# Kernel tuning notes

Measured on AMD Instinct MI355X. Metric: run time of the kernel, lower is better.

The kernel has to match this reference:

```python
import jax, jax.numpy as jnp
import numpy as np

N_NODES = 100000
N_EDGES = 1250000
D_FEAT = 64


def setup_inputs() -> dict:
    key = jax.random.key(0)
    kx, ke = jax.random.split(key)
    x = jax.random.normal(kx, (N_NODES, D_FEAT), dtype=jnp.float32)
    edge_index = jax.random.randint(ke, (2, N_EDGES), 0, N_NODES, dtype=jnp.int64)
    return {"x": x, "edge_index": edge_index}


def reference(x, edge_index):
    # propagate: scatter_nested gathers x[idxj] grouped by destination idxi
    # (a ragged per-node neighbor set); the module's sum_nested reduces each
    # group. Expressed densely and jit-ably as gather + segment-sum.
    idxi = edge_index[0, :]  # destination nodes
    idxj = edge_index[1, :]  # source nodes
    messages = x[idxj]  # [E, D] edge-level gather (memory-bound)
    out = jax.ops.segment_sum(messages, idxi, num_segments=N_NODES)  # [N, D]
    return out
```

## Files before the change

### kernel.cpp

```cpp
#include <hip/hip_runtime.h>

#define N_NODES 100000
#define N_EDGES 1250000
#define D_FEAT  64

#define NPB     256
#define NBINS   ((N_NODES + NPB - 1) / NPB)
#define BCAP    4096
#define EPB     4096
#define K1B     ((N_EDGES + EPB - 1) / EPB)
#define OVF_CAP 32768

#define CAP     48


__global__ __launch_bounds__(512) void k1_bin_kernel(
        const int* __restrict__ idxi, const int* __restrict__ idxj,
        int* __restrict__ gcursor, int* __restrict__ ovfcnt,
        int* __restrict__ ovf, int* __restrict__ binbuf) {
    __shared__ int hist[512];
    __shared__ int runstart[512];
    __shared__ int gbase[NBINS];
    __shared__ int cur[NBINS];
    __shared__ int staged[EPB];
    __shared__ unsigned short sbin[EPB];
    int t = threadIdx.x;
    hist[t] = 0;
    __syncthreads();

    long long base = (long long)blockIdx.x * EPB;
    int d[8], s[8], bn[8];
#pragma unroll
    for (int j = 0; j < 8; ++j) {
        long long e = base + t + j * 512;
        if (e < N_EDGES) {
            d[j] = idxi[e];
            s[j] = idxj[e];
            bn[j] = d[j] >> 8;
            atomicAdd(&hist[bn[j]], 1);
        } else {
            bn[j] = -1;
        }
    }
    __syncthreads();

    runstart[t] = hist[t];
    __syncthreads();
    for (int off = 1; off < 512; off <<= 1) {
        int add = (t >= off) ? runstart[t - off] : 0;
        __syncthreads();
        runstart[t] += add;
        __syncthreads();
    }
    int excl = runstart[t] - hist[t];
    __syncthreads();
    runstart[t] = excl;
    if (t < NBINS) {
        gbase[t] = hist[t] ? atomicAdd(&gcursor[t], hist[t]) : 0;
        cur[t] = 0;
    }
    __syncthreads();

#pragma unroll
    for (int j = 0; j < 8; ++j) {
        if (bn[j] >= 0) {
            int lofs = atomicAdd(&cur[bn[j]], 1);
            int idx = runstart[bn[j]] + lofs;
            staged[idx] = ((d[j] & 255) << 17) | s[j];
            sbin[idx] = (unsigned short)bn[j];
        }
    }
    __syncthreads();

    long long rem = (long long)N_EDGES - base;
    int n = (rem < EPB) ? (int)rem : EPB;
    for (int i = t; i < n; i += 512) {
        int b = sbin[i];
        int p = staged[i];
        int tgt = gbase[b] + (i - runstart[b]);
        if (tgt < BCAP) {
            binbuf[(size_t)b * BCAP + tgt] = p;
        } else {
            int op = atomicAdd(ovfcnt, 1);
            if (op < OVF_CAP) { ovf[2 * op] = b * NPB + (p >> 17); ovf[2 * op + 1] = p & 0x1FFFF; }
        }
    }
}

__global__ __launch_bounds__(1024) void k23_fused_kernel(
        const float* __restrict__ x, const int* __restrict__ gcursor,
        const int* __restrict__ binbuf, float* __restrict__ out) {
    __shared__ int cnt[NPB];
    __shared__ int excl[NPB];
    __shared__ int cur[NPB];
    __shared__ int stmp[NPB];
    __shared__ int srt[BCAP];
    int bin = blockIdx.x;
    int t = threadIdx.x;
    if (t < NPB) cnt[t] = 0;
    __syncthreads();

    int n = gcursor[bin];
    if (n > BCAP) n = BCAP;
    const int* src = binbuf + (size_t)bin * BCAP;
    int p[4];
#pragma unroll
    for (int j = 0; j < 4; ++j) {
        int i = t + j * 1024;
        p[j] = (i < n) ? src[i] : -1;
        if (p[j] >= 0) atomicAdd(&cnt[p[j] >> 17], 1);
    }
    __syncthreads();

    if (t < NPB) stmp[t] = cnt[t];
    __syncthreads();
    for (int off = 1; off < NPB; off <<= 1) {
        int v = 0;
        if (t < NPB && t >= off) v = stmp[t - off];
        __syncthreads();
        if (t < NPB) stmp[t] += v;
        __syncthreads();
    }
    if (t < NPB) {
        excl[t] = stmp[t] - cnt[t];
        cur[t] = 0;
    }
    __syncthreads();

#pragma unroll
    for (int j = 0; j < 4; ++j) {
        if (p[j] >= 0) {
            int dl = p[j] >> 17;
            int pos = excl[dl] + atomicAdd(&cur[dl], 1);
            srt[pos] = p[j] & 0x1FFFF;
        }
    }
    __syncthreads();

    int wave = t >> 6;
    int lane = t & 63;
    int sub  = lane >> 4;
    int c4   = lane & 15;
    for (int i = 0; i < 16; ++i) {
        int dloc = wave * 16 + i;
        int node = bin * NPB + dloc;
        if (node >= N_NODES) break;
        int base = excl[dloc];
        int l = cnt[dloc];
        float4 acc = make_float4(0.f, 0.f, 0.f, 0.f);
        int k = 0;
        for (; k + 8 <= l; k += 8) {
            int s0 = srt[base + k + sub];
            int s1 = srt[base + k + 4 + sub];
            const float4 v0 = *(const float4*)(x + (size_t)s0 * D_FEAT + c4 * 4);
            const float4 v1 = *(const float4*)(x + (size_t)s1 * D_FEAT + c4 * 4);
            acc.x += v0.x + v1.x;
            acc.y += v0.y + v1.y;
            acc.z += v0.z + v1.z;
            acc.w += v0.w + v1.w;
        }
        if (k + 4 <= l) {
            int s0 = srt[base + k + sub];
            const float4 v0 = *(const float4*)(x + (size_t)s0 * D_FEAT + c4 * 4);
            acc.x += v0.x; acc.y += v0.y; acc.z += v0.z; acc.w += v0.w;
            k += 4;
        }
        if (k + sub < l) {
            int s0 = srt[base + k + sub];
            const float4 v0 = *(const float4*)(x + (size_t)s0 * D_FEAT + c4 * 4);
            acc.x += v0.x; acc.y += v0.y; acc.z += v0.z; acc.w += v0.w;
        }

        acc.x += __shfl_xor(acc.x, 16, 64);
        acc.y += __shfl_xor(acc.y, 16, 64);
        acc.z += __shfl_xor(acc.z, 16, 64);
        acc.w += __shfl_xor(acc.w, 16, 64);
        acc.x += __shfl_xor(acc.x, 32, 64);
        acc.y += __shfl_xor(acc.y, 32, 64);
        acc.z += __shfl_xor(acc.z, 32, 64);
        acc.w += __shfl_xor(acc.w, 32, 64);

        if (lane < 16) {
            ((float4*)out)[(size_t)node * 16 + c4] = acc;
        }
    }
}

__global__ __launch_bounds__(256) void ovf_fixup_kernel(
        const float* __restrict__ x, const int* __restrict__ ovfcnt,
        const int* __restrict__ ovf, float* __restrict__ out) {
    int n = *ovfcnt;
    if (n > OVF_CAP) n = OVF_CAP;
    long long total = (long long)n * 16;
    long long stride = (long long)gridDim.x * blockDim.x;
    for (long long t = blockIdx.x * blockDim.x + threadIdx.x; t < total; t += stride) {
        int e  = (int)(t >> 4);
        int fo = ((int)t & 15) << 2;
        int d = ovf[2 * e];
        int s = ovf[2 * e + 1];
        const float4 v = *(const float4*)(x + (size_t)s * D_FEAT + fo);
        float* o = out + (size_t)d * D_FEAT + fo;
        atomicAdd(o + 0, v.x);
        atomicAdd(o + 1, v.y);
        atomicAdd(o + 2, v.z);
        atomicAdd(o + 3, v.w);
    }
}


__global__ __launch_bounds__(256) void scatter_pad_kernel(
        const int* __restrict__ idxi, const int* __restrict__ idxj,
        int* __restrict__ cnt, int* __restrict__ ovfcnt,
        int* __restrict__ ovf, int* __restrict__ bucket) {
    int e = blockIdx.x * blockDim.x + threadIdx.x;
    if (e >= N_EDGES) return;
    int d = idxi[e];
    int s = idxj[e];
    int pos = atomicAdd(&cnt[d], 1);
    if (pos < CAP) {
        bucket[(size_t)d * CAP + pos] = s;
    } else {
        int op = atomicAdd(ovfcnt, 1);
        if (op < OVF_CAP) { ovf[2 * op] = d; ovf[2 * op + 1] = s; }
    }
}

__global__ __launch_bounds__(256) void gather_pad_kernel(
        const float* __restrict__ x, const int* __restrict__ cnt,
        const int* __restrict__ bucket, float* __restrict__ out) {
    int node = blockIdx.x * 4 + (threadIdx.x >> 6);
    int lane = threadIdx.x & 63;
    if (node >= N_NODES) return;
    int c = cnt[node];
    if (c > CAP) c = CAP;
    const int* b = bucket + (size_t)node * CAP;
    float acc = 0.f;
    int k = 0;
    for (; k + 4 <= c; k += 4) {
        int4 s4 = *(const int4*)(b + k);
        float a0 = x[(size_t)s4.x * D_FEAT + lane];
        float a1 = x[(size_t)s4.y * D_FEAT + lane];
        float a2 = x[(size_t)s4.z * D_FEAT + lane];
        float a3 = x[(size_t)s4.w * D_FEAT + lane];
        acc += (a0 + a1) + (a2 + a3);
    }
    for (; k < c; ++k) acc += x[(size_t)b[k] * D_FEAT + lane];
    out[(size_t)node * D_FEAT + lane] = acc;
}


__global__ __launch_bounds__(256) void zero_f4_kernel(float* __restrict__ out, int n4) {
    int i = blockIdx.x * blockDim.x + threadIdx.x;
    if (i < n4) ((float4*)out)[i] = make_float4(0.f, 0.f, 0.f, 0.f);
}

__global__ __launch_bounds__(256) void scatter_add_kernel(const float* __restrict__ x,
                                                          const int* __restrict__ idxi,
                                                          const int* __restrict__ idxj,
                                                          float* __restrict__ out) {
    int t = blockIdx.x * blockDim.x + threadIdx.x;
    int e = t >> 4;
    if (e >= N_EDGES) return;
    int fo = (t & 15) << 2;
    int dst = idxi[e];
    int src = idxj[e];
    const float4 v = *(const float4*)(x + (size_t)src * D_FEAT + fo);
    float* o = out + (size_t)dst * D_FEAT + fo;
    atomicAdd(o + 0, v.x);
    atomicAdd(o + 1, v.y);
    atomicAdd(o + 2, v.z);
    atomicAdd(o + 3, v.w);
}

extern "C" void kernel_launch(void* const* d_in, const int* in_sizes, int n_in,
                              void* d_out, int out_size, void* d_ws, size_t ws_size,
                              hipStream_t stream) {
    const float* x  = (const float*)d_in[0];
    const int*   ei = (const int*)d_in[1];
    const int*   idxi = ei;
    const int*   idxj = ei + N_EDGES;
    float* out = (float*)d_out;

    int nbe = (N_EDGES + 255) / 256;
    int gather_blocks = (N_NODES + 3) / 4;

    {
        size_t need = (512 + 16 + 2 * (size_t)OVF_CAP +
                       (size_t)NBINS * BCAP) * sizeof(int);
        if (ws_size >= need) {
            int* gcursor = (int*)d_ws;
            int* ovfcnt  = gcursor + 512;
            int* ovf     = ovfcnt + 16;
            int* binbuf  = ovf + 2 * OVF_CAP;

            hipMemsetAsync(gcursor, 0, (512 + 16) * sizeof(int), stream);
            k1_bin_kernel<<<K1B, 512, 0, stream>>>(idxi, idxj, gcursor, ovfcnt, ovf, binbuf);
            k23_fused_kernel<<<NBINS, 1024, 0, stream>>>(x, gcursor, binbuf, out);
            ovf_fixup_kernel<<<16, 256, 0, stream>>>(x, ovfcnt, ovf, out);
            return;
        }
    }

    {
        size_t need = ((size_t)N_NODES + 16 + 2 * (size_t)OVF_CAP +
                       (size_t)N_NODES * CAP) * sizeof(int);
        if (ws_size >= need) {
            int* cnt    = (int*)d_ws;
            int* ovfcnt = cnt + N_NODES;
            int* ovf    = cnt + N_NODES + 16;
            int* bucket = ovf + 2 * OVF_CAP;

            hipMemsetAsync(cnt, 0, (N_NODES + 16) * sizeof(int), stream);
            scatter_pad_kernel<<<nbe, 256, 0, stream>>>(idxi, idxj, cnt, ovfcnt, ovf, bucket);
            gather_pad_kernel<<<gather_blocks, 256, 0, stream>>>(x, cnt, bucket, out);
            ovf_fixup_kernel<<<16, 256, 0, stream>>>(x, ovfcnt, ovf, out);
            return;
        }
    }

    int n4 = (N_NODES * D_FEAT) / 4;
    zero_f4_kernel<<<(n4 + 255) / 256, 256, 0, stream>>>(out, n4);
    long long total_threads = (long long)N_EDGES * 16;
    scatter_add_kernel<<<(int)((total_threads + 255) / 256), 256, 0, stream>>>(x, idxi, idxj, out);
}
```

Baseline: 141.1 us.

## Coarsen binning to 512-node superbins and gather 64-node blocks with XCD remap

The binning kernel now uses 196 coarse superbins of 512 nodes. Each thread writes directly to global memory with per-block atomic bases, which removes the shared-memory staging and prefix scan. The gather kernel runs one 256-thread block per 64-node sub-bin and filters its superbin with ballot compaction. It uses a wave-shuffle scan, remaps block IDs so adjacent blocks share an XCD, and has each 16-lane group own whole nodes, which removes the cross-lane reductions. The cost is that every gather block rereads the whole superbin (8x redundant index reads), and the direct global scatter writes are less coalesced. The pad-bucket fallback path is also removed.

```diff
diff --git a/kernel.cpp b/kernel.cpp
--- a/kernel.cpp
+++ b/kernel.cpp
@@ -4,183 +4,173 @@
 #define N_EDGES 1250000
 #define D_FEAT  64
 
-#define NPB     256
-#define NBINS   ((N_NODES + NPB - 1) / NPB)
-#define BCAP    4096
-#define EPB     4096
-#define K1B     ((N_EDGES + EPB - 1) / EPB)
-#define OVF_CAP 32768
-
-#define CAP     48
-
-
-__global__ __launch_bounds__(512) void k1_bin_kernel(
+#define SB_SHIFT 9
+#define SB_NODES 512
+#define NSB      ((N_NODES + SB_NODES - 1) / SB_NODES)
+#define SBCAP    7168
+#define OVF_CAP  32768
+
+#define K1_BLOCKS  1024
+#define K1_THREADS 512
+#define K1_STRIDE  (K1_BLOCKS * K1_THREADS)
+#define K1_ITERS   ((N_EDGES + K1_STRIDE - 1) / K1_STRIDE)
+
+#define NPB   64
+#define NBLK  ((N_NODES + NPB - 1) / NPB)
+#define KCAP  1280
+
+__global__ __launch_bounds__(K1_THREADS) void k1_bin_kernel(
         const int* __restrict__ idxi, const int* __restrict__ idxj,
         int* __restrict__ gcursor, int* __restrict__ ovfcnt,
         int* __restrict__ ovf, int* __restrict__ binbuf) {
-    __shared__ int hist[512];
-    __shared__ int runstart[512];
-    __shared__ int gbase[NBINS];
-    __shared__ int cur[NBINS];
-    __shared__ int staged[EPB];
-    __shared__ unsigned short sbin[EPB];
+    __shared__ int hist[NSB];
+    __shared__ int gbase[NSB];
+    __shared__ int cur[NSB];
     int t = threadIdx.x;
-    hist[t] = 0;
-    __syncthreads();
-
-    long long base = (long long)blockIdx.x * EPB;
-    int d[8], s[8], bn[8];
+    if (t < NSB) hist[t] = 0;
+    __syncthreads();
+
+    int dd[K1_ITERS], ss[K1_ITERS];
+    int e0 = blockIdx.x * K1_THREADS + t;
 #pragma unroll
-    for (int j = 0; j < 8; ++j) {
-        long long e = base + t + j * 512;
+    for (int j = 0; j < K1_ITERS; ++j) {
+        int e = e0 + j * K1_STRIDE;
         if (e < N_EDGES) {
-            d[j] = idxi[e];
-            s[j] = idxj[e];
-            bn[j] = d[j] >> 8;
-            atomicAdd(&hist[bn[j]], 1);
+            dd[j] = idxi[e];
+            ss[j] = idxj[e];
+            atomicAdd(&hist[dd[j] >> SB_SHIFT], 1);
         } else {
-            bn[j] = -1;
-        }
-    }
-    __syncthreads();
-
-    runstart[t] = hist[t];
-    __syncthreads();
-    for (int off = 1; off < 512; off <<= 1) {
-        int add = (t >= off) ? runstart[t - off] : 0;
-        __syncthreads();
-        runstart[t] += add;
-        __syncthreads();
-    }
-    int excl = runstart[t] - hist[t];
-    __syncthreads();
-    runstart[t] = excl;
-    if (t < NBINS) {
-        gbase[t] = hist[t] ? atomicAdd(&gcursor[t], hist[t]) : 0;
+            dd[j] = -1;
+        }
+    }
+    __syncthreads();
+
+    if (t < NSB) {
+        int h = hist[t];
+        gbase[t] = h ? atomicAdd(&gcursor[t], h) : 0;
         cur[t] = 0;
     }
     __syncthreads();
 
 #pragma unroll
-    for (int j = 0; j < 8; ++j) {
-        if (bn[j] >= 0) {
-            int lofs = atomicAdd(&cur[bn[j]], 1);
-            int idx = runstart[bn[j]] + lofs;
-            staged[idx] = ((d[j] & 255) << 17) | s[j];
-            sbin[idx] = (unsigned short)bn[j];
-        }
-    }
-    __syncthreads();
-
-    long long rem = (long long)N_EDGES - base;
-    int n = (rem < EPB) ? (int)rem : EPB;
-    for (int i = t; i < n; i += 512) {
-        int b = sbin[i];
-        int p = staged[i];
-        int tgt = gbase[b] + (i - runstart[b]);
-        if (tgt < BCAP) {
-            binbuf[(size_t)b * BCAP + tgt] = p;
-        } else {
-            int op = atomicAdd(ovfcnt, 1);
-            if (op < OVF_CAP) { ovf[2 * op] = b * NPB + (p >> 17); ovf[2 * op + 1] = p & 0x1FFFF; }
-        }
-    }
-}
-
-__global__ __launch_bounds__(1024) void k23_fused_kernel(
+    for (int j = 0; j < K1_ITERS; ++j) {
+        if (dd[j] >= 0) {
+            int b = dd[j] >> SB_SHIFT;
+            int pos = gbase[b] + atomicAdd(&cur[b], 1);
+            if (pos < SBCAP) {
+                binbuf[b * SBCAP + pos] = ((dd[j] & (SB_NODES - 1)) << 17) | ss[j];
+            } else {
+                int op = atomicAdd(ovfcnt, 1);
+                if (op < OVF_CAP) { ovf[2 * op] = dd[j]; ovf[2 * op + 1] = ss[j]; }
+            }
+        }
+    }
+}
+
+__global__ __launch_bounds__(256) void k23_gather_kernel(
         const float* __restrict__ x, const int* __restrict__ gcursor,
-        const int* __restrict__ binbuf, float* __restrict__ out) {
+        const int* __restrict__ binbuf, int* __restrict__ ovfcnt,
+        int* __restrict__ ovf, float* __restrict__ out) {
     __shared__ int cnt[NPB];
     __shared__ int excl[NPB];
     __shared__ int cur[NPB];
-    __shared__ int stmp[NPB];
-    __shared__ int srt[BCAP];
-    int bin = blockIdx.x;
+    __shared__ int klist[KCAP];
+    __shared__ int srt[KCAP];
+    __shared__ int nk;
+
+    int bid = blockIdx.x;
+    int nwg = NBLK;
+    int xcd = bid & 7;
+    int lid = bid >> 3;
+    int q = nwg >> 3, r = nwg & 7;
+    int blk = (xcd < r ? xcd * (q + 1) : r * (q + 1) + (xcd - r) * q) + lid;
+
     int t = threadIdx.x;
+    int lane = t & 63;
     if (t < NPB) cnt[t] = 0;
-    __syncthreads();
-
-    int n = gcursor[bin];
-    if (n > BCAP) n = BCAP;
-    const int* src = binbuf + (size_t)bin * BCAP;
-    int p[4];
+    if (t == 0) nk = 0;
+    __syncthreads();
+
+    int sb  = blk >> 3;
+    int my3 = blk & 7;
+    int n = gcursor[sb];
+    if (n > SBCAP) n = SBCAP;
+    const int* buf = binbuf + (size_t)sb * SBCAP;
+
+    for (int i0 = 0; i0 < n; i0 += 256) {
+        int i = i0 + t;
+        int p = (i < n) ? buf[i] : -1;
+        bool keep = (p >= 0) && ((p >> 23) == my3);
+        unsigned long long m = __ballot(keep);
+        int tot = __popcll(m);
+        int base;
+        if (lane == 0) base = atomicAdd(&nk, tot);
+        base = __shfl(base, 0, 64);
+        if (keep) {
+            int pos = base + __popcll(m & ((1ull << lane) - 1));
+            if (pos < KCAP) {
+                klist[pos] = p;
+                atomicAdd(&cnt[(p >> 17) & (NPB - 1)], 1);
+            } else {
+                int op = atomicAdd(ovfcnt, 1);
+                if (op < OVF_CAP) {
+                    ovf[2 * op]     = blk * NPB + ((p >> 17) & (NPB - 1));
+                    ovf[2 * op + 1] = p & 0x1FFFF;
+                }
+            }
+        }
+    }
+    __syncthreads();
+
+    if (t < NPB) {
+        int v = cnt[t];
+        int vinc = v;
 #pragma unroll
-    for (int j = 0; j < 4; ++j) {
-        int i = t + j * 1024;
-        p[j] = (i < n) ? src[i] : -1;
-        if (p[j] >= 0) atomicAdd(&cnt[p[j] >> 17], 1);
-    }
-    __syncthreads();
-
-    if (t < NPB) stmp[t] = cnt[t];
-    __syncthreads();
-    for (int off = 1; off < NPB; off <<= 1) {
-        int v = 0;
-        if (t < NPB && t >= off) v = stmp[t - off];
-        __syncthreads();
-        if (t < NPB) stmp[t] += v;
-        __syncthreads();
-    }
-    if (t < NPB) {
-        excl[t] = stmp[t] - cnt[t];
+        for (int off = 1; off < NPB; off <<= 1) {
+            int u = __shfl_up(vinc, off, 64);
+            if (lane >= off) vinc += u;
+        }
+        excl[t] = vinc - v;
         cur[t] = 0;
     }
     __syncthreads();
 
-#pragma unroll
-    for (int j = 0; j < 4; ++j) {
-        if (p[j] >= 0) {
-            int dl = p[j] >> 17;
-            int pos = excl[dl] + atomicAdd(&cur[dl], 1);
-            srt[pos] = p[j] & 0x1FFFF;
-        }
+    int kn = nk;
+    if (kn > KCAP) kn = KCAP;
+    for (int i = t; i < kn; i += 256) {
+        int p = klist[i];
+        int dl = (p >> 17) & (NPB - 1);
+        int pos = excl[dl] + atomicAdd(&cur[dl], 1);
+        srt[pos] = p & 0x1FFFF;
     }
     __syncthreads();
 
     int wave = t >> 6;
-    int lane = t & 63;
     int sub  = lane >> 4;
     int c4   = lane & 15;
-    for (int i = 0; i < 16; ++i) {
-        int dloc = wave * 16 + i;
-        int node = bin * NPB + dloc;
-        if (node >= N_NODES) break;
-        int base = excl[dloc];
-        int l = cnt[dloc];
+    const float4* xp = (const float4*)x;
+    for (int nd = 0; nd < 4; ++nd) {
+        int dl = wave * 16 + sub * 4 + nd;
+        int node = blk * NPB + dl;
+        int k = excl[dl];
+        int end = k + cnt[dl];
         float4 acc = make_float4(0.f, 0.f, 0.f, 0.f);
-        int k = 0;
-        for (; k + 8 <= l; k += 8) {
-            int s0 = srt[base + k + sub];
-            int s1 = srt[base + k + 4 + sub];
-            const float4 v0 = *(const float4*)(x + (size_t)s0 * D_FEAT + c4 * 4);
-            const float4 v1 = *(const float4*)(x + (size_t)s1 * D_FEAT + c4 * 4);
-            acc.x += v0.x + v1.x;
-            acc.y += v0.y + v1.y;
-            acc.z += v0.z + v1.z;
-            acc.w += v0.w + v1.w;
-        }
-        if (k + 4 <= l) {
-            int s0 = srt[base + k + sub];
-            const float4 v0 = *(const float4*)(x + (size_t)s0 * D_FEAT + c4 * 4);
+        for (; k + 4 <= end; k += 4) {
+            int s0 = srt[k], s1 = srt[k + 1], s2 = srt[k + 2], s3 = srt[k + 3];
+            float4 v0 = xp[s0 * 16 + c4];
+            float4 v1 = xp[s1 * 16 + c4];
+            float4 v2 = xp[s2 * 16 + c4];
+            float4 v3 = xp[s3 * 16 + c4];
+            acc.x += (v0.x + v1.x) + (v2.x + v3.x);
+            acc.y += (v0.y + v1.y) + (v2.y + v3.y);
+            acc.z += (v0.z + v1.z) + (v2.z + v3.z);
+            acc.w += (v0.w + v1.w) + (v2.w + v3.w);
+        }
+        for (; k < end; ++k) {
+            float4 v0 = xp[srt[k] * 16 + c4];
             acc.x += v0.x; acc.y += v0.y; acc.z += v0.z; acc.w += v0.w;
-            k += 4;
-        }
-        if (k + sub < l) {
-            int s0 = srt[base + k + sub];
-            const float4 v0 = *(const float4*)(x + (size_t)s0 * D_FEAT + c4 * 4);
-            acc.x += v0.x; acc.y += v0.y; acc.z += v0.z; acc.w += v0.w;
-        }
-
-        acc.x += __shfl_xor(acc.x, 16, 64);
-        acc.y += __shfl_xor(acc.y, 16, 64);
-        acc.z += __shfl_xor(acc.z, 16, 64);
-        acc.w += __shfl_xor(acc.w, 16, 64);
-        acc.x += __shfl_xor(acc.x, 32, 64);
-        acc.y += __shfl_xor(acc.y, 32, 64);
-        acc.z += __shfl_xor(acc.z, 32, 64);
-        acc.w += __shfl_xor(acc.w, 32, 64);
-
-        if (lane < 16) {
+        }
+        if (node < N_NODES) {
             ((float4*)out)[(size_t)node * 16 + c4] = acc;
         }
     }
@@ -208,47 +198,6 @@
 }
 
 
-__global__ __launch_bounds__(256) void scatter_pad_kernel(
-        const int* __restrict__ idxi, const int* __restrict__ idxj,
-        int* __restrict__ cnt, int* __restrict__ ovfcnt,
-        int* __restrict__ ovf, int* __restrict__ bucket) {
-    int e = blockIdx.x * blockDim.x + threadIdx.x;
-    if (e >= N_EDGES) return;
-    int d = idxi[e];
-    int s = idxj[e];
-    int pos = atomicAdd(&cnt[d], 1);
-    if (pos < CAP) {
-        bucket[(size_t)d * CAP + pos] = s;
-    } else {
-        int op = atomicAdd(ovfcnt, 1);
-        if (op < OVF_CAP) { ovf[2 * op] = d; ovf[2 * op + 1] = s; }
-    }
-}
-
-__global__ __launch_bounds__(256) void gather_pad_kernel(
-        const float* __restrict__ x, const int* __restrict__ cnt,
-        const int* __restrict__ bucket, float* __restrict__ out) {
-    int node = blockIdx.x * 4 + (threadIdx.x >> 6);
-    int lane = threadIdx.x & 63;
-    if (node >= N_NODES) return;
-    int c = cnt[node];
-    if (c > CAP) c = CAP;
-    const int* b = bucket + (size_t)node * CAP;
-    float acc = 0.f;
-    int k = 0;
-    for (; k + 4 <= c; k += 4) {
-        int4 s4 = *(const int4*)(b + k);
-        float a0 = x[(size_t)s4.x * D_FEAT + lane];
-        float a1 = x[(size_t)s4.y * D_FEAT + lane];
-        float a2 = x[(size_t)s4.z * D_FEAT + lane];
-        float a3 = x[(size_t)s4.w * D_FEAT + lane];
-        acc += (a0 + a1) + (a2 + a3);
-    }
-    for (; k < c; ++k) acc += x[(size_t)b[k] * D_FEAT + lane];
-    out[(size_t)node * D_FEAT + lane] = acc;
-}
-
-
 __global__ __launch_bounds__(256) void zero_f4_kernel(float* __restrict__ out, int n4) {
     int i = blockIdx.x * blockDim.x + threadIdx.x;
     if (i < n4) ((float4*)out)[i] = make_float4(0.f, 0.f, 0.f, 0.f);
@@ -281,38 +230,20 @@
     const int*   idxj = ei + N_EDGES;
     float* out = (float*)d_out;
 
-    int nbe = (N_EDGES + 255) / 256;
-    int gather_blocks = (N_NODES + 3) / 4;
-
     {
-        size_t need = (512 + 16 + 2 * (size_t)OVF_CAP +
-                       (size_t)NBINS * BCAP) * sizeof(int);
+        size_t need = (256 + 16 + 2 * (size_t)OVF_CAP +
+                       (size_t)NSB * SBCAP) * sizeof(int);
         if (ws_size >= need) {
             int* gcursor = (int*)d_ws;
-            int* ovfcnt  = gcursor + 512;
+            int* ovfcnt  = gcursor + 256;
             int* ovf     = ovfcnt + 16;
             int* binbuf  = ovf + 2 * OVF_CAP;
 
-            hipMemsetAsync(gcursor, 0, (512 + 16) * sizeof(int), stream);
-            k1_bin_kernel<<<K1B, 512, 0, stream>>>(idxi, idxj, gcursor, ovfcnt, ovf, binbuf);
-            k23_fused_kernel<<<NBINS, 1024, 0, stream>>>(x, gcursor, binbuf, out);
-            ovf_fixup_kernel<<<16, 256, 0, stream>>>(x, ovfcnt, ovf, out);
-            return;
-        }
-    }
-
-    {
-        size_t need = ((size_t)N_NODES + 16 + 2 * (size_t)OVF_CAP +
-                       (size_t)N_NODES * CAP) * sizeof(int);
-        if (ws_size >= need) {
-            int* cnt    = (int*)d_ws;
-            int* ovfcnt = cnt + N_NODES;
-            int* ovf    = cnt + N_NODES + 16;
-            int* bucket = ovf + 2 * OVF_CAP;
-
-            hipMemsetAsync(cnt, 0, (N_NODES + 16) * sizeof(int), stream);
-            scatter_pad_kernel<<<nbe, 256, 0, stream>>>(idxi, idxj, cnt, ovfcnt, ovf, bucket);
-            gather_pad_kernel<<<gather_blocks, 256, 0, stream>>>(x, cnt, bucket, out);
+            hipMemsetAsync(gcursor, 0, (256 + 16) * sizeof(int), stream);
+            k1_bin_kernel<<<K1_BLOCKS, K1_THREADS, 0, stream>>>(idxi, idxj, gcursor,
+                                                                ovfcnt, ovf, binbuf);
+            k23_gather_kernel<<<NBLK, 256, 0, stream>>>(x, gcursor, binbuf,
+                                                        ovfcnt, ovf, out);
             ovf_fixup_kernel<<<16, 256, 0, stream>>>(x, ovfcnt, ovf, out);
             return;
         }
```

After: 160.9 us. 1.14x slower.

## Use wave-shuffle scans and per-quarter-wave node gather without cross-lane reduction

Applied to the files above, without the earlier changes.

Both kernels replace the multi-barrier shared-memory Hillis-Steele prefix scans with a single-wavefront shuffle scan. In k1 the scan now covers only the bins in use, where it previously covered a padded 512. The gather stage now assigns one node per 16-lane group, four nodes per group in turn, instead of one node per wave. Each group walks its node's neighbour list serially with 4-way unrolled float4 loads, which removes the final shuffle reduction across groups. The unused padded-bucket fallback path is deleted. The trade-off is that load balance across lanes now depends on each node's degree, and per-group serial loops may diverge.

```diff
diff --git a/kernel.cpp b/kernel.cpp
--- a/kernel.cpp
+++ b/kernel.cpp
@@ -11,52 +11,65 @@
 #define K1B     ((N_EDGES + EPB - 1) / EPB)
 #define OVF_CAP 32768
 
-#define CAP     48
-
-
 __global__ __launch_bounds__(512) void k1_bin_kernel(
         const int* __restrict__ idxi, const int* __restrict__ idxj,
         int* __restrict__ gcursor, int* __restrict__ ovfcnt,
         int* __restrict__ ovf, int* __restrict__ binbuf) {
-    __shared__ int hist[512];
-    __shared__ int runstart[512];
+    __shared__ int hist[NBINS + 1];
+    __shared__ int runstart[NBINS + 1];
     __shared__ int gbase[NBINS];
     __shared__ int cur[NBINS];
     __shared__ int staged[EPB];
     __shared__ unsigned short sbin[EPB];
     int t = threadIdx.x;
-    hist[t] = 0;
-    __syncthreads();
-
-    long long base = (long long)blockIdx.x * EPB;
+    if (t <= NBINS) hist[t] = 0;
+    __syncthreads();
+
+    int base = blockIdx.x * EPB;
+    int n = N_EDGES - base; if (n > EPB) n = EPB;
+
     int d[8], s[8], bn[8];
 #pragma unroll
     for (int j = 0; j < 8; ++j) {
-        long long e = base + t + j * 512;
-        if (e < N_EDGES) {
-            d[j] = idxi[e];
-            s[j] = idxj[e];
-            bn[j] = d[j] >> 8;
-            atomicAdd(&hist[bn[j]], 1);
-        } else {
-            bn[j] = -1;
-        }
-    }
-    __syncthreads();
-
-    runstart[t] = hist[t];
-    __syncthreads();
-    for (int off = 1; off < 512; off <<= 1) {
-        int add = (t >= off) ? runstart[t - off] : 0;
-        __syncthreads();
-        runstart[t] += add;
-        __syncthreads();
-    }
-    int excl = runstart[t] - hist[t];
-    __syncthreads();
-    runstart[t] = excl;
+        int i = t + j * 512;
+        if (i < n) { d[j] = idxi[base + i]; s[j] = idxj[base + i]; }
+        else       { d[j] = -1; s[j] = 0; }
+    }
+#pragma unroll
+    for (int j = 0; j < 8; ++j) {
+        bn[j] = (d[j] >= 0) ? (d[j] >> 8) : -1;
+        if (bn[j] >= 0) atomicAdd(&hist[bn[j]], 1);
+    }
+    __syncthreads();
+
+    if (t < 64) {
+        int h[7];
+        int sum = 0;
+#pragma unroll
+        for (int q = 0; q < 7; ++q) {
+            int b = t * 7 + q;
+            h[q] = (b < NBINS) ? hist[b] : 0;
+            sum += h[q];
+        }
+        int inc = sum;
+#pragma unroll
+        for (int off = 1; off < 64; off <<= 1) {
+            int u = __shfl_up(inc, off, 64);
+            if (t >= off) inc += u;
+        }
+        int ex = inc - sum;
+#pragma unroll
+        for (int q = 0; q < 7; ++q) {
+            int b = t * 7 + q;
+            if (b < NBINS) runstart[b] = ex;
+            ex += h[q];
+        }
+    }
+    __syncthreads();
+
     if (t < NBINS) {
-        gbase[t] = hist[t] ? atomicAdd(&gcursor[t], hist[t]) : 0;
+        int h = hist[t];
+        gbase[t] = h ? atomicAdd(&gcursor[t], h) : 0;
         cur[t] = 0;
     }
     __syncthreads();
@@ -64,22 +77,19 @@
 #pragma unroll
     for (int j = 0; j < 8; ++j) {
         if (bn[j] >= 0) {
-            int lofs = atomicAdd(&cur[bn[j]], 1);
-            int idx = runstart[bn[j]] + lofs;
+            int idx = runstart[bn[j]] + atomicAdd(&cur[bn[j]], 1);
             staged[idx] = ((d[j] & 255) << 17) | s[j];
             sbin[idx] = (unsigned short)bn[j];
         }
     }
     __syncthreads();
 
-    long long rem = (long long)N_EDGES - base;
-    int n = (rem < EPB) ? (int)rem : EPB;
     for (int i = t; i < n; i += 512) {
         int b = sbin[i];
         int p = staged[i];
         int tgt = gbase[b] + (i - runstart[b]);
         if (tgt < BCAP) {
-            binbuf[(size_t)b * BCAP + tgt] = p;
+            binbuf[b * BCAP + tgt] = p;
         } else {
             int op = atomicAdd(ovfcnt, 1);
             if (op < OVF_CAP) { ovf[2 * op] = b * NPB + (p >> 17); ovf[2 * op + 1] = p & 0x1FFFF; }
@@ -93,7 +103,6 @@
     __shared__ int cnt[NPB];
     __shared__ int excl[NPB];
     __shared__ int cur[NPB];
-    __shared__ int stmp[NPB];
     __shared__ int srt[BCAP];
     int bin = blockIdx.x;
     int t = threadIdx.x;
@@ -103,27 +112,35 @@
     int n = gcursor[bin];
     if (n > BCAP) n = BCAP;
     const int* src = binbuf + (size_t)bin * BCAP;
+
     int p[4];
 #pragma unroll
     for (int j = 0; j < 4; ++j) {
         int i = t + j * 1024;
         p[j] = (i < n) ? src[i] : -1;
+    }
+#pragma unroll
+    for (int j = 0; j < 4; ++j)
         if (p[j] >= 0) atomicAdd(&cnt[p[j] >> 17], 1);
-    }
-    __syncthreads();
-
-    if (t < NPB) stmp[t] = cnt[t];
-    __syncthreads();
-    for (int off = 1; off < NPB; off <<= 1) {
-        int v = 0;
-        if (t < NPB && t >= off) v = stmp[t - off];
-        __syncthreads();
-        if (t < NPB) stmp[t] += v;
-        __syncthreads();
-    }
-    if (t < NPB) {
-        excl[t] = stmp[t] - cnt[t];
-        cur[t] = 0;
+    __syncthreads();
+
+    if (t < 64) {
+        int b0 = t * 4;
+        int h0 = cnt[b0], h1 = cnt[b0 + 1], h2 = cnt[b0 + 2], h3 = cnt[b0 + 3];
+        int s01 = h0 + h1;
+        int sum = s01 + h2 + h3;
+        int inc = sum;
+#pragma unroll
+        for (int off = 1; off < 64; off <<= 1) {
+            int u = __shfl_up(inc, off, 64);
+            if (t >= off) inc += u;
+        }
+        int ex = inc - sum;
+        excl[b0]     = ex;
+        excl[b0 + 1] = ex + h0;
+        excl[b0 + 2] = ex + s01;
+        excl[b0 + 3] = ex + s01 + h2;
+        cur[b0] = 0; cur[b0 + 1] = 0; cur[b0 + 2] = 0; cur[b0 + 3] = 0;
     }
     __syncthreads();
 
@@ -137,52 +154,33 @@
     }
     __syncthreads();
 
-    int wave = t >> 6;
-    int lane = t & 63;
-    int sub  = lane >> 4;
-    int c4   = lane & 15;
-    for (int i = 0; i < 16; ++i) {
-        int dloc = wave * 16 + i;
-        int node = bin * NPB + dloc;
-        if (node >= N_NODES) break;
-        int base = excl[dloc];
-        int l = cnt[dloc];
+    int w = t >> 6, lane = t & 63;
+    int sub = lane >> 4, c4 = lane & 15;
+    const float4* xp = (const float4*)x;
+#pragma unroll
+    for (int i2 = 0; i2 < 4; ++i2) {
+        int dl = w * 16 + sub * 4 + i2;
+        int node = bin * NPB + dl;
+        int k = excl[dl];
+        int end = k + cnt[dl];
         float4 acc = make_float4(0.f, 0.f, 0.f, 0.f);
-        int k = 0;
-        for (; k + 8 <= l; k += 8) {
-            int s0 = srt[base + k + sub];
-            int s1 = srt[base + k + 4 + sub];
-            const float4 v0 = *(const float4*)(x + (size_t)s0 * D_FEAT + c4 * 4);
-            const float4 v1 = *(const float4*)(x + (size_t)s1 * D_FEAT + c4 * 4);
-            acc.x += v0.x + v1.x;
-            acc.y += v0.y + v1.y;
-            acc.z += v0.z + v1.z;
-            acc.w += v0.w + v1.w;
-        }
-        if (k + 4 <= l) {
-            int s0 = srt[base + k + sub];
-            const float4 v0 = *(const float4*)(x + (size_t)s0 * D_FEAT + c4 * 4);
+        for (; k + 4 <= end; k += 4) {
+            int a0 = srt[k], a1 = srt[k + 1], a2 = srt[k + 2], a3 = srt[k + 3];
+            float4 v0 = xp[(size_t)a0 * 16 + c4];
+            float4 v1 = xp[(size_t)a1 * 16 + c4];
+            float4 v2 = xp[(size_t)a2 * 16 + c4];
+            float4 v3 = xp[(size_t)a3 * 16 + c4];
+            acc.x += (v0.x + v1.x) + (v2.x + v3.x);
+            acc.y += (v0.y + v1.y) + (v2.y + v3.y);
+            acc.z += (v0.z + v1.z) + (v2.z + v3.z);
+            acc.w += (v0.w + v1.w) + (v2.w + v3.w);
+        }
+        for (; k < end; ++k) {
+            float4 v0 = xp[(size_t)srt[k] * 16 + c4];
             acc.x += v0.x; acc.y += v0.y; acc.z += v0.z; acc.w += v0.w;
-            k += 4;
-        }
-        if (k + sub < l) {
-            int s0 = srt[base + k + sub];
-            const float4 v0 = *(const float4*)(x + (size_t)s0 * D_FEAT + c4 * 4);
-            acc.x += v0.x; acc.y += v0.y; acc.z += v0.z; acc.w += v0.w;
-        }
-
-        acc.x += __shfl_xor(acc.x, 16, 64);
-        acc.y += __shfl_xor(acc.y, 16, 64);
-        acc.z += __shfl_xor(acc.z, 16, 64);
-        acc.w += __shfl_xor(acc.w, 16, 64);
-        acc.x += __shfl_xor(acc.x, 32, 64);
-        acc.y += __shfl_xor(acc.y, 32, 64);
-        acc.z += __shfl_xor(acc.z, 32, 64);
-        acc.w += __shfl_xor(acc.w, 32, 64);
-
-        if (lane < 16) {
+        }
+        if (node < N_NODES)
             ((float4*)out)[(size_t)node * 16 + c4] = acc;
-        }
     }
 }
 
@@ -208,47 +206,6 @@
 }
 
 
-__global__ __launch_bounds__(256) void scatter_pad_kernel(
-        const int* __restrict__ idxi, const int* __restrict__ idxj,
-        int* __restrict__ cnt, int* __restrict__ ovfcnt,
-        int* __restrict__ ovf, int* __restrict__ bucket) {
-    int e = blockIdx.x * blockDim.x + threadIdx.x;
-    if (e >= N_EDGES) return;
-    int d = idxi[e];
-    int s = idxj[e];
-    int pos = atomicAdd(&cnt[d], 1);
-    if (pos < CAP) {
-        bucket[(size_t)d * CAP + pos] = s;
-    } else {
-        int op = atomicAdd(ovfcnt, 1);
-        if (op < OVF_CAP) { ovf[2 * op] = d; ovf[2 * op + 1] = s; }
-    }
-}
-
-__global__ __launch_bounds__(256) void gather_pad_kernel(
-        const float* __restrict__ x, const int* __restrict__ cnt,
-        const int* __restrict__ bucket, float* __restrict__ out) {
-    int node = blockIdx.x * 4 + (threadIdx.x >> 6);
-    int lane = threadIdx.x & 63;
-    if (node >= N_NODES) return;
-    int c = cnt[node];
-    if (c > CAP) c = CAP;
-    const int* b = bucket + (size_t)node * CAP;
-    float acc = 0.f;
-    int k = 0;
-    for (; k + 4 <= c; k += 4) {
-        int4 s4 = *(const int4*)(b + k);
-        float a0 = x[(size_t)s4.x * D_FEAT + lane];
-        float a1 = x[(size_t)s4.y * D_FEAT + lane];
-        float a2 = x[(size_t)s4.z * D_FEAT + lane];
-        float a3 = x[(size_t)s4.w * D_FEAT + lane];
-        acc += (a0 + a1) + (a2 + a3);
-    }
-    for (; k < c; ++k) acc += x[(size_t)b[k] * D_FEAT + lane];
-    out[(size_t)node * D_FEAT + lane] = acc;
-}
-
-
 __global__ __launch_bounds__(256) void zero_f4_kernel(float* __restrict__ out, int n4) {
     int i = blockIdx.x * blockDim.x + threadIdx.x;
     if (i < n4) ((float4*)out)[i] = make_float4(0.f, 0.f, 0.f, 0.f);
@@ -281,9 +238,6 @@
     const int*   idxj = ei + N_EDGES;
     float* out = (float*)d_out;
 
-    int nbe = (N_EDGES + 255) / 256;
-    int gather_blocks = (N_NODES + 3) / 4;
-
     {
         size_t need = (512 + 16 + 2 * (size_t)OVF_CAP +
                        (size_t)NBINS * BCAP) * sizeof(int);
@@ -301,23 +255,6 @@
         }
     }
 
-    {
-        size_t need = ((size_t)N_NODES + 16 + 2 * (size_t)OVF_CAP +
-                       (size_t)N_NODES * CAP) * sizeof(int);
-        if (ws_size >= need) {
-            int* cnt    = (int*)d_ws;
-            int* ovfcnt = cnt + N_NODES;
-            int* ovf    = cnt + N_NODES + 16;
-            int* bucket = ovf + 2 * OVF_CAP;
-
-            hipMemsetAsync(cnt, 0, (N_NODES + 16) * sizeof(int), stream);
-            scatter_pad_kernel<<<nbe, 256, 0, stream>>>(idxi, idxj, cnt, ovfcnt, ovf, bucket);
-            gather_pad_kernel<<<gather_blocks, 256, 0, stream>>>(x, cnt, bucket, out);
-            ovf_fixup_kernel<<<16, 256, 0, stream>>>(x, ovfcnt, ovf, out);
-            return;
-        }
-    }
-
     int n4 = (N_NODES * D_FEAT) / 4;
     zero_f4_kernel<<<(n4 + 255) / 256, 256, 0, stream>>>(out, n4);
     long long total_threads = (long long)N_EDGES * 16;
```

Measured after the change: 136.4 us. 3.4% less time.
